# Performance work log

Hardware: AMD Instinct MI355X
Metric: run time of the kernel (lower is better)

The kernel has to match this reference:

```python
import jax, jax.numpy as jnp
import numpy as np

ITER_NUM = 512
BATCH = 65536
HIDDEN = 256
DELTA_T = 0.1


def setup_inputs() -> dict:
    key = jax.random.key(0)
    k1, k2, k3, k4 = jax.random.split(key, 4)
    inflows = jax.random.uniform(k1, (ITER_NUM, BATCH, 1), dtype=jnp.float32)
    storage0 = jax.random.uniform(k2, (BATCH,), dtype=jnp.float32)
    W1 = jax.random.normal(k3, (2, HIDDEN), dtype=jnp.float32) * 0.5
    b1 = jnp.zeros((HIDDEN,), dtype=jnp.float32)
    W2 = jax.random.normal(k4, (HIDDEN, 1), dtype=jnp.float32) * 0.1
    b2 = jnp.zeros((1,), dtype=jnp.float32)
    return {"inflows": inflows, "storage0": storage0, "W1": W1, "b1": b1, "W2": W2, "b2": b2}


def reference(inflows, storage0, W1, b1, W2, b2):
    # AnnModel: Linear(nx,hidden) -> ReLU -> Linear(hidden,ny)
    def mlp(x):  # x: (B, 2)
        h = jax.nn.relu(x @ W1 + b1)          # (B, H)
        return h @ W2 + b2                     # (B, 1)

    def step(storage, inflow):  # storage: (B,1), inflow: (B,1)
        x = jnp.concatenate([inflow, storage], axis=1)      # (B, 2)
        outflow = mlp(x)                                     # (B, 1)
        storage_new = DELTA_T * (inflow - outflow) + storage # water balance update
        return storage_new, (storage_new, outflow)

    s0 = storage0[:, None]  # (B, 1)
    _, (stor_seq, outflows) = jax.lax.scan(step, s0, inflows)
    storages = jnp.concatenate([s0[None], stor_seq], axis=0)  # (T+1, B, 1)
    return storages, outflows
```

## Files before the change

### kernel.cpp

```cpp
#include <hip/hip_runtime.h>

#define DT 0.1f

typedef float v2f __attribute__((ext_vector_type(2)));

__global__ void pack_weights(const float* __restrict__ W1, const float* __restrict__ b1,
                             const float* __restrict__ W2, float4* __restrict__ ws, int hidden) {
    int j = blockIdx.x * blockDim.x + threadIdx.x;
    if (j < hidden) {
        ws[j] = make_float4(W1[j], W1[hidden + j], b1[j], W2[j]);
    }
}

__device__ __forceinline__ v2f pk_fma(v2f a, v2f b, v2f c) {
    v2f d;
    asm("v_pk_fma_f32 %0, %1, %2, %3" : "=v"(d) : "v"(a), "v"(b), "v"(c));
    return d;
}

template <int CTRL>
__device__ __forceinline__ float dpp_add(float x) {
    int v = __builtin_amdgcn_mov_dpp(__float_as_int(x), CTRL, 0xf, 0xf, true);
    return x + __int_as_float(v);
}

__global__ __launch_bounds__(256, 2) void waterbalance(
    const float* __restrict__ inflows, const float* __restrict__ storage0,
    const float4* __restrict__ ws, const float* __restrict__ b2,
    float* __restrict__ out_storages, float* __restrict__ out_outflows,
    int iters, int batch)
{
    const int tid = blockIdx.x * blockDim.x + threadIdx.x;
    const int e = tid >> 3;
    const int p = tid & 7;
    if (e >= batch) return;

    v2f wx[16], wy[16], wb[16], w2[16];
    #pragma unroll
    for (int r = 0; r < 16; ++r) {
        float4 a = ws[p * 32 + 2 * r];
        float4 b = ws[p * 32 + 2 * r + 1];
        wx[r] = (v2f){a.x, b.x};
        wy[r] = (v2f){a.y, b.y};
        wb[r] = (v2f){a.z, b.z};
        w2[r] = (v2f){a.w, b.w};
    }

    const float b2v = b2[0];

    float s = storage0[e];
    if (p == 0) out_storages[e] = s;

    const float* __restrict__ inp = inflows + e;
    float* __restrict__ po = out_outflows + e;
    float* __restrict__ ps = out_storages + (size_t)batch + e;

    const int nchunk = iters >> 2;
    const int tail_start = nchunk << 2;

    float buf[4];
    #pragma unroll
    for (int r = 0; r < 4; ++r) buf[r] = inp[(size_t)r * batch];

    for (int c = 0; c < nchunk; ++c) {
        float nb[4];
        if (c + 1 < nchunk) {
            const float* q = inp + (size_t)(c + 1) * 4 * batch;
            #pragma unroll
            for (int r = 0; r < 4; ++r) nb[r] = q[(size_t)r * batch];
        } else {
            #pragma unroll
            for (int r = 0; r < 4; ++r) nb[r] = 0.0f;
        }

        #pragma unroll
        for (int r = 0; r < 4; ++r) {
            asm("" : "+v"(wx[0]), "+v"(wx[1]), "+v"(wx[2]), "+v"(wx[3]),
                     "+v"(wx[4]), "+v"(wx[5]), "+v"(wx[6]), "+v"(wx[7]),
                     "+v"(wx[8]), "+v"(wx[9]), "+v"(wx[10]), "+v"(wx[11]),
                     "+v"(wx[12]), "+v"(wx[13]), "+v"(wx[14]), "+v"(wx[15]));
            asm("" : "+v"(wy[0]), "+v"(wy[1]), "+v"(wy[2]), "+v"(wy[3]),
                     "+v"(wy[4]), "+v"(wy[5]), "+v"(wy[6]), "+v"(wy[7]),
                     "+v"(wy[8]), "+v"(wy[9]), "+v"(wy[10]), "+v"(wy[11]),
                     "+v"(wy[12]), "+v"(wy[13]), "+v"(wy[14]), "+v"(wy[15]));
            asm("" : "+v"(wb[0]), "+v"(wb[1]), "+v"(wb[2]), "+v"(wb[3]),
                     "+v"(wb[4]), "+v"(wb[5]), "+v"(wb[6]), "+v"(wb[7]),
                     "+v"(wb[8]), "+v"(wb[9]), "+v"(wb[10]), "+v"(wb[11]),
                     "+v"(wb[12]), "+v"(wb[13]), "+v"(wb[14]), "+v"(wb[15]));
            asm("" : "+v"(w2[0]), "+v"(w2[1]), "+v"(w2[2]), "+v"(w2[3]),
                     "+v"(w2[4]), "+v"(w2[5]), "+v"(w2[6]), "+v"(w2[7]),
                     "+v"(w2[8]), "+v"(w2[9]), "+v"(w2[10]), "+v"(w2[11]),
                     "+v"(w2[12]), "+v"(w2[13]), "+v"(w2[14]), "+v"(w2[15]));

            const float inflow = buf[r];
            const v2f in2 = (v2f){inflow, inflow};
            const v2f s2  = (v2f){s, s};
            const v2f zero2 = (v2f)(0.0f);
            v2f acc0 = (v2f)(0.0f);
            v2f acc1 = (v2f)(0.0f);

            #pragma unroll
            for (int g = 0; g < 16; g += 2) {
                v2f z0 = pk_fma(in2, wx[g], pk_fma(s2, wy[g], wb[g]));
                z0 = __builtin_elementwise_max(z0, zero2);
                acc0 = pk_fma(z0, w2[g], acc0);

                v2f z1 = pk_fma(in2, wx[g + 1], pk_fma(s2, wy[g + 1], wb[g + 1]));
                z1 = __builtin_elementwise_max(z1, zero2);
                acc1 = pk_fma(z1, w2[g + 1], acc1);
            }

            float part = (acc0.x + acc1.x) + (acc0.y + acc1.y);
            part = dpp_add<0xB1>(part);
            part = dpp_add<0x4E>(part);
            part = dpp_add<0x141>(part);
            const float outflow = part + b2v;

            s = fmaf(DT, inflow - outflow, s);

            if (p == 0) {
                *po = outflow;
                *ps = s;
            }
            po += batch;
            ps += batch;
        }

        #pragma unroll
        for (int r = 0; r < 4; ++r) buf[r] = nb[r];
    }

    for (int t = tail_start; t < iters; ++t) {
        const float inflow = inp[(size_t)t * batch];
        const v2f in2 = (v2f){inflow, inflow};
        const v2f s2  = (v2f){s, s};
        const v2f zero2 = (v2f)(0.0f);
        v2f acc0 = (v2f)(0.0f), acc1 = (v2f)(0.0f);
        #pragma unroll
        for (int g = 0; g < 16; g += 2) {
            v2f z0 = pk_fma(in2, wx[g], pk_fma(s2, wy[g], wb[g]));
            z0 = __builtin_elementwise_max(z0, zero2);
            acc0 = pk_fma(z0, w2[g], acc0);
            v2f z1 = pk_fma(in2, wx[g + 1], pk_fma(s2, wy[g + 1], wb[g + 1]));
            z1 = __builtin_elementwise_max(z1, zero2);
            acc1 = pk_fma(z1, w2[g + 1], acc1);
        }
        float part = (acc0.x + acc1.x) + (acc0.y + acc1.y);
        part = dpp_add<0xB1>(part);
        part = dpp_add<0x4E>(part);
        part = dpp_add<0x141>(part);
        const float outflow = part + b2v;
        s = fmaf(DT, inflow - outflow, s);
        if (p == 0) {
            *po = outflow;
            *ps = s;
        }
        po += batch;
        ps += batch;
    }
}

extern "C" void kernel_launch(void* const* d_in, const int* in_sizes, int n_in,
                              void* d_out, int out_size, void* d_ws, size_t ws_size,
                              hipStream_t stream) {
    const float* inflows  = (const float*)d_in[0];
    const float* storage0 = (const float*)d_in[1];
    const float* W1       = (const float*)d_in[2];
    const float* b1       = (const float*)d_in[3];
    const float* W2       = (const float*)d_in[4];
    const float* b2       = (const float*)d_in[5];

    int batch  = in_sizes[1];
    int iters  = in_sizes[0] / batch;
    int hidden = in_sizes[3];

    float4* ws = (float4*)d_ws;
    pack_weights<<<(hidden + 255) / 256, 256, 0, stream>>>(W1, b1, W2, ws, hidden);

    float* out_storages = (float*)d_out;
    float* out_outflows = out_storages + (size_t)(iters + 1) * batch;

    int threads = batch * 8;
    waterbalance<<<(threads + 255) / 256, 256, 0, stream>>>(
        inflows, storage0, ws, b2, out_storages, out_outflows, iters, batch);
}
```

Measured before the change: 1.140 ms.

## Split each batch element across 16 lanes instead of 8

Each batch element's 256 hidden units are now spread over 16 lanes, 16 units per lane, instead of 8 lanes. This halves per-thread weight registers and the serial packed-FMA chain per time step. Launch bounds are raised to allow 4 blocks per CU, and one more DPP row-mirror step is added to reduce across 16 lanes. The per-step barrier asm on the weights is replaced by a one-time register pin, and the accumulator merge now uses a packed add. The trade-off is twice as many waves, so reduction, broadcast, load and store overhead per element roughly doubles, in exchange for shorter dependency chains and more latency hiding.

```diff
diff --git a/kernel.cpp b/kernel.cpp
--- a/kernel.cpp
+++ b/kernel.cpp
@@ -17,6 +17,11 @@
     asm("v_pk_fma_f32 %0, %1, %2, %3" : "=v"(d) : "v"(a), "v"(b), "v"(c));
     return d;
 }
+__device__ __forceinline__ v2f pk_add(v2f a, v2f b) {
+    v2f d;
+    asm("v_pk_add_f32 %0, %1, %2" : "=v"(d) : "v"(a), "v"(b));
+    return d;
+}
 
 template <int CTRL>
 __device__ __forceinline__ float dpp_add(float x) {
@@ -24,26 +29,30 @@
     return x + __int_as_float(v);
 }
 
-__global__ __launch_bounds__(256, 2) void waterbalance(
+__global__ __launch_bounds__(256, 4) void waterbalance(
     const float* __restrict__ inflows, const float* __restrict__ storage0,
     const float4* __restrict__ ws, const float* __restrict__ b2,
     float* __restrict__ out_storages, float* __restrict__ out_outflows,
     int iters, int batch)
 {
     const int tid = blockIdx.x * blockDim.x + threadIdx.x;
-    const int e = tid >> 3;
-    const int p = tid & 7;
+    const int e = tid >> 4;
+    const int p = tid & 15;
     if (e >= batch) return;
 
-    v2f wx[16], wy[16], wb[16], w2[16];
+    v2f wx[8], wy[8], wb[8], w2[8];
     #pragma unroll
-    for (int r = 0; r < 16; ++r) {
-        float4 a = ws[p * 32 + 2 * r];
-        float4 b = ws[p * 32 + 2 * r + 1];
+    for (int r = 0; r < 8; ++r) {
+        float4 a = ws[p * 16 + 2 * r];
+        float4 b = ws[p * 16 + 2 * r + 1];
         wx[r] = (v2f){a.x, b.x};
         wy[r] = (v2f){a.y, b.y};
         wb[r] = (v2f){a.z, b.z};
         w2[r] = (v2f){a.w, b.w};
+    }
+    #pragma unroll
+    for (int r = 0; r < 8; ++r) {
+        asm("" : "+v"(wx[r]), "+v"(wy[r]), "+v"(wb[r]), "+v"(w2[r]));
     }
 
     const float b2v = b2[0];
@@ -75,23 +84,6 @@
 
         #pragma unroll
         for (int r = 0; r < 4; ++r) {
-            asm("" : "+v"(wx[0]), "+v"(wx[1]), "+v"(wx[2]), "+v"(wx[3]),
-                     "+v"(wx[4]), "+v"(wx[5]), "+v"(wx[6]), "+v"(wx[7]),
-                     "+v"(wx[8]), "+v"(wx[9]), "+v"(wx[10]), "+v"(wx[11]),
-                     "+v"(wx[12]), "+v"(wx[13]), "+v"(wx[14]), "+v"(wx[15]));
-            asm("" : "+v"(wy[0]), "+v"(wy[1]), "+v"(wy[2]), "+v"(wy[3]),
-                     "+v"(wy[4]), "+v"(wy[5]), "+v"(wy[6]), "+v"(wy[7]),
-                     "+v"(wy[8]), "+v"(wy[9]), "+v"(wy[10]), "+v"(wy[11]),
-                     "+v"(wy[12]), "+v"(wy[13]), "+v"(wy[14]), "+v"(wy[15]));
-            asm("" : "+v"(wb[0]), "+v"(wb[1]), "+v"(wb[2]), "+v"(wb[3]),
-                     "+v"(wb[4]), "+v"(wb[5]), "+v"(wb[6]), "+v"(wb[7]),
-                     "+v"(wb[8]), "+v"(wb[9]), "+v"(wb[10]), "+v"(wb[11]),
-                     "+v"(wb[12]), "+v"(wb[13]), "+v"(wb[14]), "+v"(wb[15]));
-            asm("" : "+v"(w2[0]), "+v"(w2[1]), "+v"(w2[2]), "+v"(w2[3]),
-                     "+v"(w2[4]), "+v"(w2[5]), "+v"(w2[6]), "+v"(w2[7]),
-                     "+v"(w2[8]), "+v"(w2[9]), "+v"(w2[10]), "+v"(w2[11]),
-                     "+v"(w2[12]), "+v"(w2[13]), "+v"(w2[14]), "+v"(w2[15]));
-
             const float inflow = buf[r];
             const v2f in2 = (v2f){inflow, inflow};
             const v2f s2  = (v2f){s, s};
@@ -100,7 +92,7 @@
             v2f acc1 = (v2f)(0.0f);
 
             #pragma unroll
-            for (int g = 0; g < 16; g += 2) {
+            for (int g = 0; g < 8; g += 2) {
                 v2f z0 = pk_fma(in2, wx[g], pk_fma(s2, wy[g], wb[g]));
                 z0 = __builtin_elementwise_max(z0, zero2);
                 acc0 = pk_fma(z0, w2[g], acc0);
@@ -110,10 +102,12 @@
                 acc1 = pk_fma(z1, w2[g + 1], acc1);
             }
 
-            float part = (acc0.x + acc1.x) + (acc0.y + acc1.y);
+            v2f accs = pk_add(acc0, acc1);
+            float part = accs.x + accs.y;
             part = dpp_add<0xB1>(part);
             part = dpp_add<0x4E>(part);
             part = dpp_add<0x141>(part);
+            part = dpp_add<0x140>(part);
             const float outflow = part + b2v;
 
             s = fmaf(DT, inflow - outflow, s);
@@ -137,7 +131,7 @@
         const v2f zero2 = (v2f)(0.0f);
         v2f acc0 = (v2f)(0.0f), acc1 = (v2f)(0.0f);
         #pragma unroll
-        for (int g = 0; g < 16; g += 2) {
+        for (int g = 0; g < 8; g += 2) {
             v2f z0 = pk_fma(in2, wx[g], pk_fma(s2, wy[g], wb[g]));
             z0 = __builtin_elementwise_max(z0, zero2);
             acc0 = pk_fma(z0, w2[g], acc0);
@@ -145,10 +139,12 @@
             z1 = __builtin_elementwise_max(z1, zero2);
             acc1 = pk_fma(z1, w2[g + 1], acc1);
         }
-        float part = (acc0.x + acc1.x) + (acc0.y + acc1.y);
+        v2f accs = pk_add(acc0, acc1);
+        float part = accs.x + accs.y;
         part = dpp_add<0xB1>(part);
         part = dpp_add<0x4E>(part);
         part = dpp_add<0x141>(part);
+        part = dpp_add<0x140>(part);
         const float outflow = part + b2v;
         s = fmaf(DT, inflow - outflow, s);
         if (p == 0) {
@@ -180,7 +176,7 @@
     float* out_storages = (float*)d_out;
     float* out_outflows = out_storages + (size_t)(iters + 1) * batch;
 
-    int threads = batch * 8;
-    waterbalance<<<(threads + 255) / 256, 256, 0, stream>>>(
+    long long threads = (long long)batch * 16;
+    waterbalance<<<(int)((threads + 255) / 256), 256, 0, stream>>>(
         inflows, storage0, ws, b2, out_storages, out_outflows, iters, batch);
 }
```

Result: faster. 1.064 ms (-6.6%).
